# Optimization experiments

Measured on AMD Instinct MI355X. Metric: run time of the kernel, lower is better.

Reference implementation:

```python
import jax, jax.numpy as jnp
import numpy as np

C, N, NC, E, D, R = 16, 10000, 2000, 50000, 256, 32
NBLK = 3
IN_DIM = 4 + 134 + 6 * 4 + 18 * 4  # 234
EPS = 1e-5


def _instance_norm(x):
    # InstanceNorm1d (affine=False): normalize over the node axis per (config, channel)
    mu = jnp.mean(x, axis=1, keepdims=True)
    var = jnp.var(x, axis=1, keepdims=True)
    return (x - mu) * jax.lax.rsqrt(var + EPS)


def _channel_attn(x, W1, b1, W2, b2):
    t = jax.nn.relu(x @ W1 + b1)
    return jax.nn.sigmoid(t @ W2 + b2) * x


def setup_inputs() -> dict:
    key = jax.random.key(0)
    ks = jax.random.split(key, 24)
    sc = 0.05
    inp = {}
    inp["x_node_cfg"] = jax.random.randint(ks[0], (C, NC, 18), 0, 6)
    inp["x_feat"] = jax.random.normal(ks[1], (N, 134), jnp.float32)
    inp["x_node_layout_feat"] = jax.random.randint(ks[2], (N, 6), 0, 6)
    inp["x_op"] = jax.random.randint(ks[3], (N,), 0, 120)
    inp["edge_index"] = jax.random.randint(ks[4], (2, E), 0, N)
    inp["node_config_ids"] = jnp.arange(NC)
    # parameters
    inp["emb_op"] = jax.random.normal(ks[5], (120, 4)) * 0.1
    inp["emb_layout"] = jax.random.normal(ks[6], (8, 4)) * 0.1
    inp["lin1_W"] = jax.random.normal(ks[7], (IN_DIM, D)) * sc
    inp["lin1_b"] = jnp.full((D,), 0.01, jnp.float32)
    inp["ca1_W1"] = jax.random.normal(ks[8], (D, R)) * sc
    inp["ca1_b1"] = jnp.zeros((R,), jnp.float32)
    inp["ca1_W2"] = jax.random.normal(ks[9], (R, D)) * sc
    inp["ca1_b2"] = jnp.zeros((D,), jnp.float32)
    inp["lin2_W"] = jax.random.normal(ks[10], (D, D)) * sc
    inp["lin2_b"] = jnp.full((D,), 0.01, jnp.float32)
    inp["ca2_W1"] = jax.random.normal(ks[11], (D, R)) * sc
    inp["ca2_b1"] = jnp.zeros((R,), jnp.float32)
    inp["ca2_W2"] = jax.random.normal(ks[12], (R, D)) * sc
    inp["ca2_b2"] = jnp.zeros((D,), jnp.float32)
    inp["sage_Wl"] = jax.random.normal(ks[13], (NBLK, D, D)) * sc
    inp["sage_bl"] = jnp.zeros((NBLK, D), jnp.float32)
    inp["sage_Wr"] = jax.random.normal(ks[14], (NBLK, D, D)) * sc
    inp["sca_W1"] = jax.random.normal(ks[15], (NBLK, D, R)) * sc
    inp["sca_b1"] = jnp.zeros((NBLK, R), jnp.float32)
    inp["sca_W2"] = jax.random.normal(ks[16], (NBLK, R, D)) * sc
    inp["sca_b2"] = jnp.zeros((NBLK, D), jnp.float32)
    inp["cls_W"] = jax.random.normal(ks[17], (D, 1)) * sc
    inp["cls_b"] = jnp.zeros((1,), jnp.float32)
    return inp


def _forward(x_node_cfg, x_feat, x_node_layout_feat, x_op, edge_index, node_config_ids,
             emb_op, emb_layout, lin1_W, lin1_b, ca1_W1, ca1_b1, ca1_W2, ca1_b2,
             lin2_W, lin2_b, ca2_W1, ca2_b1, ca2_W2, ca2_b2,
             sage_Wl, sage_bl, sage_Wr, sca_W1, sca_b1, sca_W2, sca_b2, cls_W, cls_b):
    n_cfg = x_node_cfg.shape[0]
    n_nodes = x_feat.shape[0]
    # build per-node config feature: -2 fill, scatter configured nodes, shift by +2
    node_cfg = jnp.full((n_cfg, n_nodes, 18), -2, x_node_cfg.dtype)
    node_cfg = node_cfg.at[:, node_config_ids].set(x_node_cfg) + 2
    cfg_emb = emb_layout[node_cfg].reshape(n_cfg, n_nodes, 18 * 4)  # [C,N,72]
    layout_emb = emb_layout[x_node_layout_feat + 2].reshape(n_nodes, 6 * 4)  # [N,24]
    op_emb = emb_op[x_op]  # [N,4]
    feat = jnp.concatenate([
        jnp.broadcast_to(x_feat[None], (n_cfg, n_nodes, x_feat.shape[1])),
        cfg_emb,
        jnp.broadcast_to(layout_emb[None], (n_cfg, n_nodes, layout_emb.shape[1])),
        jnp.broadcast_to(op_emb[None], (n_cfg, n_nodes, op_emb.shape[1])),
    ], axis=2)  # [C,N,234]

    # LinearActNorm 1
    h = feat @ lin1_W + lin1_b
    h = _instance_norm(h)
    h = _channel_attn(h, ca1_W1, ca1_b1, ca1_W2, ca1_b2)
    h = jax.nn.gelu(h, approximate=False)
    # LinearActNorm 2
    h = h @ lin2_W + lin2_b
    h = _instance_norm(h)
    h = _channel_attn(h, ca2_W1, ca2_b1, ca2_W2, ca2_b2)
    h = jax.nn.gelu(h, approximate=False)

    src, tgt = edge_index[0], edge_index[1]
    cnt = jnp.zeros((n_nodes,), h.dtype).at[tgt].add(1.0)
    inv_cnt = (1.0 / jnp.maximum(cnt, 1.0))[None, :, None]
    for i in range(sage_Wl.shape[0]):
        shortcut = h
        x = _instance_norm(h)
        # SAGEConv: mean aggregation of source features at targets + root transform
        agg = jnp.zeros_like(x).at[:, tgt, :].add(x[:, src, :]) * inv_cnt
        x = agg @ sage_Wl[i] + sage_bl[i] + x @ sage_Wr[i]
        x = _channel_attn(x, sca_W1[i], sca_b1[i], sca_W2[i], sca_b2[i])
        h = jax.nn.gelu(x + shortcut, approximate=False)

    pooled = h.mean(axis=1)  # [C,D]
    return (pooled @ cls_W + cls_b).reshape(-1)  # [C]


def reference(x_node_cfg, x_feat, x_node_layout_feat, x_op, edge_index, node_config_ids,
              emb_op, emb_layout, lin1_W, lin1_b, ca1_W1, ca1_b1, ca1_W2, ca1_b2,
              lin2_W, lin2_b, ca2_W1, ca2_b1, ca2_W2, ca2_b2,
              sage_Wl, sage_bl, sage_Wr, sca_W1, sca_b1, sca_W2, sca_b2, cls_W, cls_b):
    return _forward(x_node_cfg, x_feat, x_node_layout_feat, x_op, edge_index, node_config_ids,
                    emb_op, emb_layout, lin1_W, lin1_b, ca1_W1, ca1_b1, ca1_W2, ca1_b2,
                    lin2_W, lin2_b, ca2_W1, ca2_b1, ca2_W2, ca2_b2,
                    sage_Wl, sage_bl, sage_Wr, sca_W1, sca_b1, sca_W2, sca_b2, cls_W, cls_b)
```

## Files before the change

### kernel.cpp

```cpp
#include <hip/hip_runtime.h>
#include <hip/hip_bf16.h>
#include <math.h>

constexpr int C_  = 16;
constexpr int N_  = 10000;
constexpr int NC_ = 2000;
constexpr int E_  = 50000;
constexpr int D_  = 256;
constexpr int SZ_ = N_ * D_;
constexpr float EPS_ = 1e-5f;

typedef unsigned short u16;
typedef __attribute__((ext_vector_type(8))) unsigned short us8v;
typedef __attribute__((ext_vector_type(4))) unsigned short us4v;
typedef __attribute__((ext_vector_type(8))) short s16x8;
typedef __attribute__((ext_vector_type(4))) float f32x4;

typedef __attribute__((address_space(3))) unsigned int lds_uint;
typedef const __attribute__((address_space(1))) unsigned int glb_uint;

__device__ __forceinline__ u16 f2bf(float f) {
    __hip_bfloat16 h = __float2bfloat16(f);
    return __builtin_bit_cast(u16, h);
}
__device__ __forceinline__ float bf2f(u16 h) {
    return __uint_as_float(((unsigned)h) << 16);
}
__device__ __forceinline__ float gelu_f(float x) {
    float z = x * 0.70710678118654752f;
    float az = fabsf(z);
    float t = 1.f / fmaf(0.3275911f, az, 1.f);
    float p = t * (0.254829592f + t * (-0.284496736f + t * (1.421413741f +
              t * (-1.453152027f + t * 1.061405429f))));
    float e = p * __expf(-z * z);
    float erfv = (z >= 0.f) ? (1.f - e) : (e - 1.f);
    return 0.5f * x * (1.f + erfv);
}


__global__ __launch_bounds__(256) void tbl_k(const float* __restrict__ embL,
                                             const float* __restrict__ W,
                                             float* __restrict__ T) {
    int b = blockIdx.x;
    int s = b >> 3, i = b & 7, d = threadIdx.x;
    float acc = 0.f;
#pragma unroll
    for (int k = 0; k < 4; ++k)
        acc = fmaf(embL[i * 4 + k], W[(134 + s * 4 + k) * 256 + d], acc);
    T[(s * 8 + i) * 256 + d] = acc;
}

__global__ __launch_bounds__(256) void csum_k(const float* __restrict__ T,
                                              float* __restrict__ cs) {
    int d = threadIdx.x;
    float a = 0.f;
#pragma unroll
    for (int s = 0; s < 18; ++s) a += T[(s * 8) * 256 + d];
    cs[d] = a;
}

__global__ __launch_bounds__(192) void feat_k(const float* __restrict__ xf,
                                              const int* __restrict__ xlay,
                                              const int* __restrict__ xop,
                                              const float* __restrict__ embL,
                                              const float* __restrict__ embO,
                                              float* __restrict__ f) {
    int n = blockIdx.x, j = threadIdx.x;
    if (j >= 176) return;
    float v;
    if (j < 134) v = xf[n * 134 + j];
    else if (j < 158) { int q = j - 134; int t = q >> 2, k = q & 3; v = embL[(xlay[n * 6 + t] + 2) * 4 + k]; }
    else if (j < 162) { int k = j - 158; v = embO[xop[n] * 4 + k]; }
    else v = 0.f;
    f[n * 176 + j] = v;
}

__global__ __launch_bounds__(256) void wpack_k(const float* __restrict__ W,
                                               float* __restrict__ Wp) {
    int j = blockIdx.x, d = threadIdx.x;
    float v = 0.f;
    if (j < 134) v = W[j * 256 + d];
    else if (j < 158) v = W[(206 + j - 134) * 256 + d];
    else if (j < 162) v = W[(230 + j - 158) * 256 + d];
    Wp[j * 256 + d] = v;
}

__global__ __launch_bounds__(256) void packw1_k(const float* __restrict__ W1,
                                                u16* __restrict__ dst) {
    int i = blockIdx.x * 256 + threadIdx.x;
    int j = i & 7, lane = (i >> 3) & 63, half = (i >> 9) & 1, ks = (i >> 10) & 1, wid = (i >> 11) & 3;
    int k = wid * 64 + ks * 32 + ((lane >> 4) << 3) + j;
    int col = half * 16 + (lane & 15);
    dst[i] = f2bf(W1[k * 32 + col]);
}
__global__ __launch_bounds__(256) void packw2_k(const float* __restrict__ W2,
                                                u16* __restrict__ dst) {
    int i = blockIdx.x * 256 + threadIdx.x;
    int j = i & 7, lane = (i >> 3) & 63, q = (i >> 9) & 3, wid = (i >> 11) & 3;
    int kq = lane >> 4, cl = lane & 15;
    dst[i] = f2bf(W2[(kq * 8 + j) * 256 + (wid * 4 + q) * 16 + cl]);
}

__global__ __launch_bounds__(256) void cfgpos_k(const int* __restrict__ ncid,
                                                int* __restrict__ cfgpos) {
    int i = blockIdx.x * 256 + threadIdx.x;
    if (i < NC_) cfgpos[ncid[i]] = i;
}

__global__ __launch_bounds__(256) void hist_k(const int* __restrict__ ei, int* __restrict__ cnt) {
    int e = blockIdx.x * 256 + threadIdx.x;
    if (e < E_) atomicAdd(&cnt[ei[E_ + e]], 1);
}

__global__ __launch_bounds__(1024) void scan_k(const int* __restrict__ cnt,
                                               int* __restrict__ off,
                                               int* __restrict__ cursor,
                                               float* __restrict__ invcnt) {
    __shared__ int s[1024];
    int t = threadIdx.x;
    int base = t * 10;
    int local[10];
    int part = 0;
#pragma unroll
    for (int k = 0; k < 10; ++k) {
        int idx = base + k;
        int v = (idx < N_) ? cnt[idx] : 0;
        local[k] = v; part += v;
    }
    s[t] = part;
    __syncthreads();
    for (int o = 1; o < 1024; o <<= 1) {
        int val = (t >= o) ? s[t - o] : 0;
        __syncthreads();
        s[t] += val;
        __syncthreads();
    }
    int pre = s[t] - part;
#pragma unroll
    for (int k = 0; k < 10; ++k) {
        int idx = base + k;
        if (idx < N_) {
            off[idx] = pre;
            cursor[idx] = pre;
            invcnt[idx] = 1.0f / (float)(local[k] > 1 ? local[k] : 1);
            pre += local[k];
        }
    }
    if (t == 1023) off[N_] = s[1023];
}

__global__ __launch_bounds__(256) void fill_k(const int* __restrict__ ei,
                                              int* __restrict__ cursor,
                                              int* __restrict__ csr) {
    int e = blockIdx.x * 256 + threadIdx.x;
    if (e < E_) {
        int t = ei[E_ + e];
        int p = atomicAdd(&cursor[t], 1);
        csr[p] = ei[e];
    }
}

__global__ __launch_bounds__(256) void wt2_k(const float* __restrict__ W,
                                             u16* __restrict__ Wt) {
    int j = blockIdx.x, k = threadIdx.x;
    Wt[j * 256 + k] = f2bf(W[k * 256 + j]);
}

__global__ __launch_bounds__(256) void foldw_k(const float* __restrict__ Wl,
                                               const float* __restrict__ Wr,
                                               const float* __restrict__ bl,
                                               const float* __restrict__ mu,
                                               const float* __restrict__ rs,
                                               u16* __restrict__ Wt,
                                               float* __restrict__ biasF) {
    __shared__ float red[256];
    int c = blockIdx.y, j = blockIdx.x, k = threadIdx.x;
    float rsv = rs[c * 256 + k], muv = mu[c * 256 + k];
    float fl = rsv * Wl[k * 256 + j];
    float fr = rsv * Wr[k * 256 + j];
    size_t wb = ((size_t)c * 256 + j) * 512;
    Wt[wb + k] = f2bf(fl);
    Wt[wb + 256 + k] = f2bf(fr);
    red[k] = muv * (fl + fr);
    __syncthreads();
    for (int s = 128; s > 0; s >>= 1) {
        if (k < s) red[k] += red[k + s];
        __syncthreads();
    }
    if (k == 0) biasF[c * 256 + j] = bl[j] - red[0];
}

__global__ __launch_bounds__(256) void lin1_cfg_k(const float* __restrict__ base,
                                                  const float* __restrict__ T,
                                                  const int* __restrict__ ncid,
                                                  const int* __restrict__ xcfg,
                                                  u16* __restrict__ H,
                                                  float* __restrict__ ssum,
                                                  float* __restrict__ ssq) {
    __shared__ int idxs[16][18];
    __shared__ int nid[16];
    const int c = blockIdx.z, j0 = blockIdx.x * 16, tid = threadIdx.x;
    if (tid < 16) nid[tid] = ncid[j0 + tid];
    for (int t = tid; t < 288; t += 256) {
        int row = t / 18, s = t - row * 18;
        idxs[row][s] = (xcfg[((size_t)c * NC_ + j0 + row) * 18 + s] + 2) * 256;
    }
    __syncthreads();
    const int d = tid;
    float psum = 0.f, psq = 0.f;
    for (int g = 0; g < 16; g += 4) {
        float acc[4];
#pragma unroll
        for (int gg = 0; gg < 4; ++gg) acc[gg] = base[(size_t)nid[g + gg] * 256 + d];
#pragma unroll
        for (int s = 0; s < 18; ++s) {
            const float* Ts = &T[s * 2048 + d];
#pragma unroll
            for (int gg = 0; gg < 4; ++gg)
                acc[gg] += Ts[idxs[g + gg][s]];
        }
#pragma unroll
        for (int gg = 0; gg < 4; ++gg) {
            H[((size_t)c * N_ + nid[g + gg]) * 256 + d] = f2bf(acc[gg]);
            psum += acc[gg]; psq += acc[gg] * acc[gg];
        }
    }
    atomicAdd(&ssum[c * 256 + d], psum);
    atomicAdd(&ssq[c * 256 + d], psq);
}

__global__ __launch_bounds__(256) void lin1_unc_k(const float* __restrict__ base,
                                                  const float* __restrict__ csum,
                                                  const int* __restrict__ cfgpos,
                                                  int nc,
                                                  u16* __restrict__ H,
                                                  float* __restrict__ ssum,
                                                  float* __restrict__ ssq) {
    __shared__ float red[2048];
    const int n0 = blockIdx.x * 16, tid = threadIdx.x;
    float ps[8] = {0, 0, 0, 0, 0, 0, 0, 0}, pq[8] = {0, 0, 0, 0, 0, 0, 0, 0};
#pragma unroll
    for (int it = 0; it < 2; ++it) {
        const int flat = tid + it * 256;
        const int row = flat >> 5, cb = (flat & 31) * 8;
        const int n = n0 + row;
        if (cfgpos[n] >= 0) continue;
        us8v b;
#pragma unroll
        for (int j = 0; j < 8; ++j) {
            float v = base[(size_t)n * 256 + cb + j] + csum[cb + j];
            b[j] = f2bf(v);
            ps[j] += v; pq[j] += v * v;
        }
        for (int c = 0; c < nc; ++c)
            *(us8v*)&H[((size_t)c * N_ + n) * 256 + cb] = b;
    }
#pragma unroll
    for (int j = 0; j < 8; ++j)
        red[((tid >> 5) * 32 + (tid & 31)) * 8 + j] = ps[j];
    __syncthreads();
    {
        const int cb2 = tid >> 3, j2 = tid & 7;
        float s = 0.f;
#pragma unroll
        for (int r8 = 0; r8 < 8; ++r8) s += red[(r8 * 32 + cb2) * 8 + j2];
        for (int c = 0; c < nc; ++c) atomicAdd(&ssum[c * 256 + tid], s);
    }
    __syncthreads();
#pragma unroll
    for (int j = 0; j < 8; ++j)
        red[((tid >> 5) * 32 + (tid & 31)) * 8 + j] = pq[j];
    __syncthreads();
    {
        const int cb2 = tid >> 3, j2 = tid & 7;
        float s = 0.f;
#pragma unroll
        for (int r8 = 0; r8 < 8; ++r8) s += red[(r8 * 32 + cb2) * 8 + j2];
        for (int c = 0; c < nc; ++c) atomicAdd(&ssq[c * 256 + tid], s);
    }
}

__global__ __launch_bounds__(256) void finstat_k(const float* __restrict__ ssum,
                                                 const float* __restrict__ ssq,
                                                 float* __restrict__ mu,
                                                 float* __restrict__ rs,
                                                 float* __restrict__ mrs) {
    int i = blockIdx.x * 256 + threadIdx.x;
    float m = ssum[i] * (1.0f / (float)N_);
    float v = ssq[i] * (1.0f / (float)N_) - m * m;
    float r = rsqrtf(v + EPS_);
    mu[i] = m;
    rs[i] = r;
    mrs[i] = m * r;
}

__global__ __launch_bounds__(256) void agg_k(const u16* __restrict__ H,
                                             const int* __restrict__ off,
                                             const int* __restrict__ csr,
                                             const float* __restrict__ invcnt,
                                             const float* __restrict__ mu,
                                             u16* __restrict__ Agg) {
    int wave = threadIdx.x >> 6, lane = threadIdx.x & 63;
    int pair = blockIdx.x * 4 + wave;
    int c = pair / N_, t = pair - c * N_;
    int d4 = lane * 4;
    int o0 = off[t], o1 = off[t + 1];
    int deg = o1 - o0;
    us4v o;
    if (deg > 0) {
        int myidx = (lane < deg) ? csr[o0 + lane] : 0;
        const u16* Hc = H + (size_t)c * SZ_ + d4;
        float ax = 0.f, ay = 0.f, az = 0.f, aw = 0.f;
        int lim = deg < 64 ? deg : 64;
        int i = 0;
        for (; i + 4 <= lim; i += 4) {
            int s0 = __shfl(myidx, i), s1 = __shfl(myidx, i + 1);
            int s2 = __shfl(myidx, i + 2), s3 = __shfl(myidx, i + 3);
            us4v h0 = *(const us4v*)&Hc[(size_t)s0 * 256];
            us4v h1 = *(const us4v*)&Hc[(size_t)s1 * 256];
            us4v h2 = *(const us4v*)&Hc[(size_t)s2 * 256];
            us4v h3 = *(const us4v*)&Hc[(size_t)s3 * 256];
            ax += (bf2f(h0.x) + bf2f(h1.x)) + (bf2f(h2.x) + bf2f(h3.x));
            ay += (bf2f(h0.y) + bf2f(h1.y)) + (bf2f(h2.y) + bf2f(h3.y));
            az += (bf2f(h0.z) + bf2f(h1.z)) + (bf2f(h2.z) + bf2f(h3.z));
            aw += (bf2f(h0.w) + bf2f(h1.w)) + (bf2f(h2.w) + bf2f(h3.w));
        }
        for (; i < lim; ++i) {
            int s = __shfl(myidx, i);
            us4v h = *(const us4v*)&Hc[(size_t)s * 256];
            ax += bf2f(h.x); ay += bf2f(h.y); az += bf2f(h.z); aw += bf2f(h.w);
        }
        for (int j = o0 + 64; j < o1; ++j) {
            int s = csr[j];
            us4v h = *(const us4v*)&Hc[(size_t)s * 256];
            ax += bf2f(h.x); ay += bf2f(h.y); az += bf2f(h.z); aw += bf2f(h.w);
        }
        float inv = invcnt[t];
        o.x = f2bf(ax * inv); o.y = f2bf(ay * inv);
        o.z = f2bf(az * inv); o.w = f2bf(aw * inv);
    } else {
        o.x = f2bf(mu[c * 256 + d4 + 0]);
        o.y = f2bf(mu[c * 256 + d4 + 1]);
        o.z = f2bf(mu[c * 256 + d4 + 2]);
        o.w = f2bf(mu[c * 256 + d4 + 3]);
    }
    *(us4v*)&Agg[((size_t)c * N_ + t) * 256 + d4] = o;
}

template <int STATS>
__global__ __launch_bounds__(256) void mgemm_k(
    const u16* __restrict__ A1, size_t sA1,
    const u16* __restrict__ A2, size_t sA2,
    const u16* __restrict__ Wt, size_t sW, int K1, int Ktot,
    const float* __restrict__ bias, size_t sBias,
    u16* __restrict__ Y, size_t sY, int Mrows,
    float* __restrict__ ssum, float* __restrict__ ssq)
{
    __shared__ u16 Asm[128 * 64];
    __shared__ u16 Bsm[128 * 64];
    const int tid = threadIdx.x;
    const int lane = tid & 63, wid = tid >> 6;
    const int wr = wid >> 1, wc = wid & 1;

    const int gx = gridDim.x, gy = gridDim.y;
    int nwg = gx * gy * gridDim.z;
    int orig = blockIdx.x + gx * (blockIdx.y + gy * blockIdx.z);
    int q = nwg >> 3, r = nwg & 7;
    int xcd = orig & 7, idx = orig >> 3;
    int swz = (xcd < r ? xcd * (q + 1) : r * (q + 1) + (xcd - r) * q) + idx;
    const int bx = swz % gx;
    const int tmp = swz / gx;
    const int by = tmp % gy;
    const int c  = tmp / gy;

    const int rowbase = by * 128, colbase = bx * 128;

    const u16* A1p = A1 + (size_t)c * sA1;
    const u16* A2p = A2 ? (A2 + (size_t)c * sA2) : nullptr;
    const u16* Wp  = Wt + (size_t)c * sW;

    f32x4 acc[4][4];
#pragma unroll
    for (int i = 0; i < 4; ++i)
#pragma unroll
        for (int j = 0; j < 4; ++j) acc[i][j] = (f32x4)0.f;

    const int lrow = lane >> 3;
    const int lchunk = lane & 7;

    for (int k0 = 0; k0 < Ktot; k0 += 64) {
        const u16* asrc; int ak;
        if (k0 < K1) { asrc = A1p; ak = k0; } else { asrc = A2p; ak = k0 - K1; }
#pragma unroll
        for (int i = 0; i < 4; ++i) {
            const int row = (wid * 4 + i) * 8 + lrow;
            const int srcchunk = lchunk ^ (row & 7);
            int garow = rowbase + row;
            if (garow >= Mrows) garow = Mrows - 1;
            const u16* ga = asrc + (size_t)garow * 256 + ak + srcchunk * 8;
            __builtin_amdgcn_global_load_lds((glb_uint*)ga,
                (lds_uint*)(Asm + (wid * 4 + i) * 512), 16, 0, 0);
            const u16* gb = Wp + (size_t)(colbase + row) * Ktot + k0 + srcchunk * 8;
            __builtin_amdgcn_global_load_lds((glb_uint*)gb,
                (lds_uint*)(Bsm + (wid * 4 + i) * 512), 16, 0, 0);
        }
        __syncthreads();
#pragma unroll
        for (int ks = 0; ks < 2; ++ks) {
            s16x8 aF[4], bF[4];
            const int kk = ks * 32 + ((lane >> 4) << 3);
#pragma unroll
            for (int f = 0; f < 4; ++f) {
                int ar = wr * 64 + f * 16 + (lane & 15);
                aF[f] = *(const s16x8*)&Asm[(ar * 64 + kk) ^ ((ar & 7) << 3)];
                int br = wc * 64 + f * 16 + (lane & 15);
                bF[f] = *(const s16x8*)&Bsm[(br * 64 + kk) ^ ((br & 7) << 3)];
            }
#pragma unroll
            for (int fr = 0; fr < 4; ++fr)
#pragma unroll
                for (int fc = 0; fc < 4; ++fc)
                    acc[fr][fc] = __builtin_amdgcn_mfma_f32_16x16x32_bf16(
                        aF[fr], bF[fc], acc[fr][fc], 0, 0, 0);
        }
        __syncthreads();
    }

    float bcol[4];
#pragma unroll
    for (int fc = 0; fc < 4; ++fc)
        bcol[fc] = bias[(size_t)c * sBias + colbase + wc * 64 + fc * 16 + (lane & 15)];
    u16* Yp = Y + (size_t)c * sY;
    float ps[4] = {0, 0, 0, 0}, pq[4] = {0, 0, 0, 0};
#pragma unroll
    for (int fr = 0; fr < 4; ++fr) {
#pragma unroll
        for (int i = 0; i < 4; ++i) {
            int grow = rowbase + wr * 64 + fr * 16 + ((lane >> 4) << 2) + i;
            if (grow < Mrows) {
                size_t rb = (size_t)grow * 256 + colbase + wc * 64 + (lane & 15);
#pragma unroll
                for (int fc = 0; fc < 4; ++fc) {
                    float v = acc[fr][fc][i] + bcol[fc];
                    Yp[rb + fc * 16] = f2bf(v);
                    if (STATS) { ps[fc] += v; pq[fc] += v * v; }
                }
            }
        }
    }
    if (STATS) {
#pragma unroll
        for (int fc = 0; fc < 4; ++fc) {
            float s = ps[fc], q2 = pq[fc];
            s += __shfl_xor(s, 16); s += __shfl_xor(s, 32);
            q2 += __shfl_xor(q2, 16); q2 += __shfl_xor(q2, 32);
            if (lane < 16) {
                int col = colbase + wc * 64 + fc * 16 + lane;
                atomicAdd(&ssum[c * 256 + col], s);
                atomicAdd(&ssq[c * 256 + col], q2);
            }
        }
    }
}

template <int SMODE>
__global__ __launch_bounds__(512) void msage_k(
    const u16* __restrict__ A1,
    const u16* __restrict__ A2,
    const u16* __restrict__ Wt, size_t sW,
    const float* __restrict__ biasF,
    const u16* __restrict__ W1p, const float* __restrict__ b1,
    const u16* __restrict__ W2p, const float* __restrict__ b2,
    u16* __restrict__ Yout, int Mrows,
    float* __restrict__ ssum, float* __restrict__ ssq)
{
    __shared__ __align__(16) char SM[81920];
    u16*   xbf = (u16*)SM;
    u16*   tbf = (u16*)(SM + 33792);
    float* red = (float*)SM;

    const int tid = threadIdx.x;
    const int lane = tid & 63, w = tid >> 6;
    const int cl = lane & 15, kq = lane >> 4;

    int nwg = gridDim.x * gridDim.y;
    int orig = blockIdx.x + gridDim.x * blockIdx.y;
    int q = nwg >> 3, r = nwg & 7;
    int xcd = orig & 7, idx = orig >> 3;
    int swz = (xcd < r ? xcd * (q + 1) : r * (q + 1) + (xcd - r) * q) + idx;
    const int by = swz % gridDim.x;
    const int c  = swz / gridDim.x;
    const int rowbase = by * 64;

    const u16* A1p = A1 + (size_t)c * SZ_;
    const u16* A2p = A2 + (size_t)c * SZ_;
    const u16* Wp  = Wt + (size_t)c * sW;

    f32x4 acc[4][2];
#pragma unroll
    for (int i = 0; i < 4; ++i)
#pragma unroll
        for (int j = 0; j < 2; ++j) acc[i][j] = (f32x4)0.f;

    auto stage = [&](int buf, int k0) {
        const u16* asrc = (k0 < 256) ? A1p : A2p;
        const int ak = (k0 < 256) ? k0 : (k0 - 256);
        u16* Ab = (u16*)(SM + buf * 40960);
        u16* Bb = (u16*)(SM + buf * 40960 + 8192);
        {
            const int u = tid;
            const int row = u >> 3, chunk = u & 7;
            const int sc2 = chunk ^ (row & 7);
            int garow = rowbase + row;
            if (garow >= Mrows) garow = Mrows - 1;
            __builtin_amdgcn_global_load_lds(
                (glb_uint*)(asrc + (size_t)garow * 256 + ak + sc2 * 8),
                (lds_uint*)(Ab + (w * 64) * 8), 16, 0, 0);
        }
#pragma unroll
        for (int jj = 0; jj < 4; ++jj) {
            const int u = tid + jj * 512;
            const int wcol = u >> 3, chunk = u & 7;
            const int sc2 = chunk ^ (wcol & 7);
            __builtin_amdgcn_global_load_lds(
                (glb_uint*)(Wp + (size_t)wcol * 512 + k0 + sc2 * 8),
                (lds_uint*)(Bb + (jj * 512 + w * 64) * 8), 16, 0, 0);
        }
    };

    stage(0, 0);
    __syncthreads();
    int cur = 0;
    for (int t = 0; t < 8; ++t) {
        if (t < 7) stage(cur ^ 1, (t + 1) * 64);
        const u16* Asm = (const u16*)(SM + cur * 40960);
        const u16* Bsm = (const u16*)(SM + cur * 40960 + 8192);
#pragma unroll
        for (int ks = 0; ks < 2; ++ks) {
            s16x8 aF[4], bF[2];
            const int kk = ks * 32 + kq * 8;
#pragma unroll
            for (int f = 0; f < 4; ++f) {
                const int ar = f * 16 + cl;
                aF[f] = *(const s16x8*)&Asm[(ar * 64 + kk) ^ ((ar & 7) << 3)];
            }
#pragma unroll
            for (int fc = 0; fc < 2; ++fc) {
                const int bc = w * 32 + fc * 16 + cl;
                bF[fc] = *(const s16x8*)&Bsm[(bc * 64 + kk) ^ ((bc & 7) << 3)];
            }
#pragma unroll
            for (int fr = 0; fr < 4; ++fr)
#pragma unroll
                for (int fc = 0; fc < 2; ++fc)
                    acc[fr][fc] = __builtin_amdgcn_mfma_f32_16x16x32_bf16(
                        aF[fr], bF[fc], acc[fr][fc], 0, 0, 0);
        }
        __syncthreads();
        cur ^= 1;
    }

    float bcol[2];
#pragma unroll
    for (int fc = 0; fc < 2; ++fc)
        bcol[fc] = biasF[c * 256 + w * 32 + fc * 16 + cl];

#pragma unroll
    for (int fr = 0; fr < 4; ++fr)
#pragma unroll
        for (int i = 0; i < 4; ++i) {
            const int rloc = fr * 16 + kq * 4 + i;
#pragma unroll
            for (int fc = 0; fc < 2; ++fc)
                xbf[rloc * 264 + w * 32 + fc * 16 + cl] =
                    f2bf(acc[fr][fc][i] + bcol[fc]);
        }
    __syncthreads();
    {
        const int rb = w >> 1, ch = w & 1;
        f32x4 at = (f32x4)0.f;
#pragma unroll
        for (int s = 0; s < 8; ++s) {
            s16x8 aF = *(const s16x8*)&xbf[(rb * 16 + cl) * 264 + s * 32 + kq * 8];
            s16x8 bF = *(const s16x8*)&W1p[((s * 2 + ch) * 64 + lane) * 8];
            at = __builtin_amdgcn_mfma_f32_16x16x32_bf16(aF, bF, at, 0, 0, 0);
        }
        const float b1v = b1[ch * 16 + cl];
#pragma unroll
        for (int i = 0; i < 4; ++i)
            tbf[(rb * 16 + kq * 4 + i) * 40 + ch * 16 + cl] =
                f2bf(fmaxf(at[i] + b1v, 0.f));
    }
    __syncthreads();
    {
        s16x8 aF[4];
#pragma unroll
        for (int rg = 0; rg < 4; ++rg)
            aF[rg] = *(const s16x8*)&tbf[(rg * 16 + cl) * 40 + kq * 8];
#pragma unroll
        for (int q2 = 0; q2 < 2; ++q2) {
            const int cf = w * 2 + q2;
            const int colb = cf * 16;
            s16x8 bF = *(const s16x8*)&W2p[(cf * 64 + lane) * 8];
            const float b2v = b2[colb + cl];
#pragma unroll
            for (int rg = 0; rg < 4; ++rg) {
                f32x4 a2 = __builtin_amdgcn_mfma_f32_16x16x32_bf16(
                    aF[rg], bF, (f32x4)0.f, 0, 0, 0);
#pragma unroll
                for (int i = 0; i < 4; ++i) {
                    const int ea = (rg * 16 + kq * 4 + i) * 264 + colb + cl;
                    float s = a2[i] + b2v;
                    float sig = 1.f / (1.f + __expf(-s));
                    xbf[ea] = f2bf(sig * bf2f(xbf[ea]));
                }
            }
        }
    }
    __syncthreads();
    float ps[8] = {0, 0, 0, 0, 0, 0, 0, 0}, pq[8] = {0, 0, 0, 0, 0, 0, 0, 0};
#pragma unroll
    for (int it = 0; it < 4; ++it) {
        const int e = tid + it * 512;
        const int row = e >> 5, cb = (e & 31) * 8;
        const int grow = rowbase + row;
        if (grow < Mrows) {
            us8v xv = *(const us8v*)&xbf[row * 264 + cb];
            us8v rv = *(const us8v*)&Yout[((size_t)c * N_ + grow) * 256 + cb];
            us8v ov;
#pragma unroll
            for (int j = 0; j < 8; ++j) {
                float v = gelu_f(bf2f(xv[j]) + bf2f(rv[j]));
                ov[j] = f2bf(v);
                ps[j] += v;
                if (SMODE == 1) pq[j] += v * v;
            }
            *(us8v*)&Yout[((size_t)c * N_ + grow) * 256 + cb] = ov;
        }
    }
    __syncthreads();
#pragma unroll
    for (int j = 0; j < 8; ++j)
        red[((tid >> 5) * 32 + (tid & 31)) * 8 + j] = ps[j];
    __syncthreads();
    if (tid < 256) {
        const int cb2 = tid >> 3, j2 = tid & 7;
        float s = 0.f;
#pragma unroll
        for (int r16 = 0; r16 < 16; ++r16) s += red[(r16 * 32 + cb2) * 8 + j2];
        atomicAdd(&ssum[c * 256 + cb2 * 8 + j2], s);
    }
    if (SMODE == 1) {
        __syncthreads();
#pragma unroll
        for (int j = 0; j < 8; ++j)
            red[((tid >> 5) * 32 + (tid & 31)) * 8 + j] = pq[j];
        __syncthreads();
        if (tid < 256) {
            const int cb2 = tid >> 3, j2 = tid & 7;
            float s = 0.f;
#pragma unroll
            for (int r16 = 0; r16 < 16; ++r16) s += red[(r16 * 32 + cb2) * 8 + j2];
            atomicAdd(&ssq[c * 256 + cb2 * 8 + j2], s);
        }
    }
}

__global__ __launch_bounds__(256) void gemm_k(const float* __restrict__ A1, int lda1,
                                              const float* __restrict__ W1, int K1,
                                              const float* __restrict__ bias,
                                              float* __restrict__ Y, int Mrows) {
    __shared__ float As[16][132];
    __shared__ float Bs[16][132];
    float acc[8][8];
#pragma unroll
    for (int i = 0; i < 8; ++i)
#pragma unroll
        for (int j = 0; j < 8; ++j) acc[i][j] = 0.f;

    const int tid = threadIdx.x;
    const int tr = tid >> 4, tc = tid & 15;
    const int rowbase = blockIdx.y * 128, colbase = blockIdx.x * 128;

    for (int k0 = 0; k0 < K1; k0 += 16) {
#pragma unroll
        for (int ii = 0; ii < 2; ++ii) {
            int i = tid + ii * 256;
            int rr = i >> 2, qq = i & 3;
            int grow = rowbase + rr;
            float4 vv = make_float4(0.f, 0.f, 0.f, 0.f);
            if (grow < Mrows) vv = *(const float4*)&A1[(size_t)grow * lda1 + k0 + qq * 4];
            As[qq * 4 + 0][rr] = vv.x;
            As[qq * 4 + 1][rr] = vv.y;
            As[qq * 4 + 2][rr] = vv.z;
            As[qq * 4 + 3][rr] = vv.w;
        }
#pragma unroll
        for (int ii = 0; ii < 2; ++ii) {
            int i = tid + ii * 256;
            int rr = i >> 5, qq = i & 31;
            float4 vv = *(const float4*)&W1[(size_t)(k0 + rr) * 256 + colbase + qq * 4];
            *(float4*)&Bs[rr][qq * 4] = vv;
        }
        __syncthreads();
#pragma unroll
        for (int kk = 0; kk < 16; ++kk) {
            float a[8], b[8];
            *(float4*)&a[0] = *(const float4*)&As[kk][tr * 4];
            *(float4*)&a[4] = *(const float4*)&As[kk][64 + tr * 4];
            *(float4*)&b[0] = *(const float4*)&Bs[kk][tc * 4];
            *(float4*)&b[4] = *(const float4*)&Bs[kk][64 + tc * 4];
#pragma unroll
            for (int i = 0; i < 8; ++i)
#pragma unroll
                for (int j = 0; j < 8; ++j)
                    acc[i][j] = fmaf(a[i], b[j], acc[i][j]);
        }
        __syncthreads();
    }

    float4 blo = *(const float4*)&bias[colbase + tc * 4];
    float4 bhi = *(const float4*)&bias[colbase + 64 + tc * 4];
    float bb[8] = {blo.x, blo.y, blo.z, blo.w, bhi.x, bhi.y, bhi.z, bhi.w};
#pragma unroll
    for (int i = 0; i < 8; ++i)
#pragma unroll
        for (int j = 0; j < 8; ++j) acc[i][j] += bb[j];

#pragma unroll
    for (int i = 0; i < 8; ++i) {
        int lrow = (i < 4) ? (tr * 4 + i) : (64 + tr * 4 + (i - 4));
        int grow = rowbase + lrow;
        if (grow < Mrows) {
            *(float4*)&Y[(size_t)grow * 256 + colbase + tc * 4] =
                make_float4(acc[i][0], acc[i][1], acc[i][2], acc[i][3]);
            *(float4*)&Y[(size_t)grow * 256 + colbase + 64 + tc * 4] =
                make_float4(acc[i][4], acc[i][5], acc[i][6], acc[i][7]);
        }
    }
}

template <int NORM, int RES, int SMODE>
__global__ __launch_bounds__(512) void apply_k(const u16* __restrict__ Yin,
                                               u16* __restrict__ Hout,
                                               const u16* __restrict__ Hsc,
                                               const u16* __restrict__ W1p,
                                               const float* __restrict__ b1,
                                               const u16* __restrict__ W2p,
                                               const float* __restrict__ b2,
                                               const float* __restrict__ rs,
                                               const float* __restrict__ mrs,
                                               float* __restrict__ ssum,
                                               float* __restrict__ ssq) {
    __shared__ u16 vbf[16 * 264];
    __shared__ u16 scs[(RES ? 16 : 1) * 264];
    __shared__ float tpart[8 * 528];
    __shared__ u16 tbf[16 * 40];
    __shared__ float srs[NORM ? 256 : 1], smrs[NORM ? 256 : 1];
    const int c = blockIdx.z, n0 = blockIdx.x * 16, tid = threadIdx.x;
    const int lane = tid & 63, wid = tid >> 6;
    const size_t rowbase = ((size_t)c * N_ + n0) * 256;

    if (NORM && tid < 256) { srs[tid] = rs[c * 256 + tid]; smrs[tid] = mrs[c * 256 + tid]; }
    {
        const int row = tid >> 5, cb = (tid & 31) * 8;
        us8v x = *(const us8v*)&Yin[rowbase + row * 256 + cb];
        us8v r;
        if (RES) r = *(const us8v*)&Hsc[rowbase + row * 256 + cb];
        if (NORM) {
            __syncthreads();
            us8v y;
#pragma unroll
            for (int j = 0; j < 8; ++j)
                y[j] = f2bf(fmaf(bf2f(x[j]), srs[cb + j], -smrs[cb + j]));
            *(us8v*)&vbf[row * 264 + cb] = y;
        } else {
            *(us8v*)&vbf[row * 264 + cb] = x;
        }
        if (RES) *(us8v*)&scs[row * 264 + cb] = r;
    }
    __syncthreads();

    {
        const int arow = lane & 15, kq = lane >> 4;
        const int k = wid * 32 + kq * 8;
        s16x8 aF = *(const s16x8*)&vbf[arow * 264 + k];
        s16x8 bF0 = *(const s16x8*)&W1p[((wid * 2 + 0) * 64 + lane) * 8];
        s16x8 bF1 = *(const s16x8*)&W1p[((wid * 2 + 1) * 64 + lane) * 8];
        f32x4 at0 = __builtin_amdgcn_mfma_f32_16x16x32_bf16(aF, bF0, (f32x4)0.f, 0, 0, 0);
        f32x4 at1 = __builtin_amdgcn_mfma_f32_16x16x32_bf16(aF, bF1, (f32x4)0.f, 0, 0, 0);
#pragma unroll
        for (int i = 0; i < 4; ++i) {
            tpart[wid * 528 + (kq * 4 + i) * 33 + (lane & 15)] = at0[i];
            tpart[wid * 528 + (kq * 4 + i) * 33 + 16 + (lane & 15)] = at1[i];
        }
    }
    __syncthreads();

    {
        const int nr = tid >> 5, col = tid & 31;
        float s = b1[col];
#pragma unroll
        for (int w8 = 0; w8 < 8; ++w8)
            s += tpart[w8 * 528 + nr * 33 + col];
        tbf[nr * 40 + col] = f2bf(fmaxf(s, 0.f));
    }
    __syncthreads();

    {
        const int cl = lane & 15, kq = lane >> 4;
        s16x8 aF = *(const s16x8*)&tbf[cl * 40 + kq * 8];
        float ps[2] = {0, 0}, pq[2] = {0, 0};
#pragma unroll
        for (int q = 0; q < 2; ++q) {
            const int colb = (wid * 2 + q) * 16;
            s16x8 bF = *(const s16x8*)&W2p[((wid * 2 + q) * 64 + lane) * 8];
            f32x4 acc = __builtin_amdgcn_mfma_f32_16x16x32_bf16(aF, bF, (f32x4)0.f, 0, 0, 0);
            const float b2v = b2[colb + cl];
#pragma unroll
            for (int i = 0; i < 4; ++i) {
                const int row = kq * 4 + i;
                const int ea = row * 264 + colb + cl;
                float s = acc[i] + b2v;
                float sig = 1.0f / (1.0f + __expf(-s));
                float val = sig * bf2f(vbf[ea]);
                if (RES) val += bf2f(scs[ea]);
                val = gelu_f(val);
                vbf[ea] = f2bf(val);
                if (SMODE) { ps[q] += val; if (SMODE == 1) pq[q] += val * val; }
            }
        }
        if (SMODE) {
#pragma unroll
            for (int q = 0; q < 2; ++q) {
                float s = ps[q];
                s += __shfl_xor(s, 16); s += __shfl_xor(s, 32);
                if (SMODE == 1) {
                    float q2 = pq[q];
                    q2 += __shfl_xor(q2, 16); q2 += __shfl_xor(q2, 32);
                    if (lane < 16) atomicAdd(&ssq[c * 256 + (wid * 2 + q) * 16 + lane], q2);
                }
                if (lane < 16) atomicAdd(&ssum[c * 256 + (wid * 2 + q) * 16 + lane], s);
            }
        }
    }
    __syncthreads();

    {
        const int row = tid >> 5, cb = (tid & 31) * 8;
        us8v h = *(const us8v*)&vbf[row * 264 + cb];
        *(us8v*)&Hout[rowbase + row * 256 + cb] = h;
    }
}

__global__ __launch_bounds__(256) void cls_k(const float* __restrict__ pooled_sum,
                                             const float* __restrict__ clsW,
                                             const float* __restrict__ clsb,
                                             float* __restrict__ out) {
    __shared__ float red[256];
    int c = blockIdx.x, d = threadIdx.x;
    red[d] = pooled_sum[c * 256 + d] * (1.0f / (float)N_) * clsW[d];
    __syncthreads();
    for (int s = 128; s > 0; s >>= 1) {
        if (d < s) red[d] += red[d + s];
        __syncthreads();
    }
    if (d == 0) out[c] = red[0] + clsb[0];
}

static inline size_t alup(size_t x) { return (x + 255) & ~(size_t)255; }

extern "C" void kernel_launch(void* const* d_in, const int* in_sizes, int n_in,
                              void* d_out, int out_size, void* d_ws, size_t ws_size,
                              hipStream_t stream) {
    const int*   xcfg   = (const int*)d_in[0];
    const float* xfeat  = (const float*)d_in[1];
    const int*   xlay   = (const int*)d_in[2];
    const int*   xop    = (const int*)d_in[3];
    const int*   ei     = (const int*)d_in[4];
    const int*   ncid   = (const int*)d_in[5];
    const float* embO   = (const float*)d_in[6];
    const float* embL   = (const float*)d_in[7];
    const float* lin1W  = (const float*)d_in[8];
    const float* lin1b  = (const float*)d_in[9];
    const float* ca1W1  = (const float*)d_in[10];
    const float* ca1b1  = (const float*)d_in[11];
    const float* ca1W2  = (const float*)d_in[12];
    const float* ca1b2  = (const float*)d_in[13];
    const float* lin2W  = (const float*)d_in[14];
    const float* lin2b  = (const float*)d_in[15];
    const float* ca2W1  = (const float*)d_in[16];
    const float* ca2b1  = (const float*)d_in[17];
    const float* ca2W2  = (const float*)d_in[18];
    const float* ca2b2  = (const float*)d_in[19];
    const float* sageWl = (const float*)d_in[20];
    const float* sagebl = (const float*)d_in[21];
    const float* sageWr = (const float*)d_in[22];
    const float* scaW1  = (const float*)d_in[23];
    const float* scab1  = (const float*)d_in[24];
    const float* scaW2  = (const float*)d_in[25];
    const float* scab2  = (const float*)d_in[26];
    const float* clsW   = (const float*)d_in[27];
    const float* clsb   = (const float*)d_in[28];
    float* out = (float*)d_out;

    char* w = (char*)d_ws;
    size_t o = 0;
    auto take = [&](size_t bytes) { char* p = w + o; o = alup(o + bytes); return p; };
    float* base    = (float*)take((size_t)N_ * 256 * 4);
    float* feat162 = (float*)take((size_t)N_ * 176 * 4);
    float* W162    = (float*)take((size_t)176 * 256 * 4);
    float* T       = (float*)take((size_t)18 * 8 * 256 * 4);
    float* csum    = (float*)take((size_t)256 * 4);
    float* stats   = (float*)take((size_t)6 * 8192 * 4);
    float* MU      = (float*)take((size_t)5 * 4096 * 4);
    float* RS      = (float*)take((size_t)5 * 4096 * 4);
    float* MRS     = (float*)take((size_t)5 * 4096 * 4);
    float* invcnt  = (float*)take((size_t)N_ * 4);
    int*   cnt     = (int*)take((size_t)N_ * 4);
    int*   off     = (int*)take((size_t)(N_ + 1) * 4);
    int*   cursor  = (int*)take((size_t)N_ * 4);
    int*   csr     = (int*)take((size_t)E_ * 4);
    int*   cfgpos  = (int*)take((size_t)N_ * 4);
    u16*   Wt2     = (u16*)take((size_t)256 * 256 * 2);
    u16*   Wfold   = (u16*)take((size_t)C_ * 256 * 512 * 2);
    float* biasF   = (float*)take((size_t)C_ * 256 * 4);
    u16*   CAW1    = (u16*)take((size_t)5 * 8192 * 2);
    u16*   CAW2    = (u16*)take((size_t)5 * 8192 * 2);

    const size_t slab = (size_t)SZ_ * 2;
    size_t avail = (ws_size > o) ? (ws_size - o) : 0;
    int Cc = (int)(avail / (3 * slab + 768));
    if (Cc > C_) Cc = C_;
    if (Cc < 1) Cc = 1;
    u16* BufH = (u16*)take((size_t)Cc * slab);
    u16* BufY = (u16*)take((size_t)Cc * slab);
    u16* BufA = (u16*)take((size_t)Cc * slab);
    (void)in_sizes; (void)n_in; (void)out_size;

    auto S = [&](int s) { return stats + (size_t)s * 8192; };
    auto Q = [&](int s) { return stats + (size_t)s * 8192 + 4096; };

    hipMemsetAsync(stats, 0, 6 * 8192 * 4, stream);
    hipMemsetAsync(cnt, 0, N_ * 4, stream);
    hipMemsetAsync(cfgpos, 0xFF, N_ * 4, stream);

    tbl_k<<<144, 256, 0, stream>>>(embL, lin1W, T);
    csum_k<<<1, 256, 0, stream>>>(T, csum);
    feat_k<<<N_, 192, 0, stream>>>(xfeat, xlay, xop, embL, embO, feat162);
    wpack_k<<<176, 256, 0, stream>>>(lin1W, W162);
    wt2_k<<<256, 256, 0, stream>>>(lin2W, Wt2);
    packw1_k<<<32, 256, 0, stream>>>(ca1W1, CAW1 + 0 * 8192);
    packw1_k<<<32, 256, 0, stream>>>(ca2W1, CAW1 + 1 * 8192);
    packw1_k<<<32, 256, 0, stream>>>(scaW1 + 0 * 8192, CAW1 + 2 * 8192);
    packw1_k<<<32, 256, 0, stream>>>(scaW1 + 1 * 8192, CAW1 + 3 * 8192);
    packw1_k<<<32, 256, 0, stream>>>(scaW1 + 2 * 8192, CAW1 + 4 * 8192);
    packw2_k<<<32, 256, 0, stream>>>(ca1W2, CAW2 + 0 * 8192);
    packw2_k<<<32, 256, 0, stream>>>(ca2W2, CAW2 + 1 * 8192);
    packw2_k<<<32, 256, 0, stream>>>(scaW2 + 0 * 8192, CAW2 + 2 * 8192);
    packw2_k<<<32, 256, 0, stream>>>(scaW2 + 1 * 8192, CAW2 + 3 * 8192);
    packw2_k<<<32, 256, 0, stream>>>(scaW2 + 2 * 8192, CAW2 + 4 * 8192);
    cfgpos_k<<<(NC_ + 255) / 256, 256, 0, stream>>>(ncid, cfgpos);
    hist_k<<<(E_ + 255) / 256, 256, 0, stream>>>(ei, cnt);
    scan_k<<<1, 1024, 0, stream>>>(cnt, off, cursor, invcnt);
    fill_k<<<(E_ + 255) / 256, 256, 0, stream>>>(ei, cursor, csr);

    gemm_k<<<dim3(2, 79, 1), 256, 0, stream>>>(feat162, 176, W162, 176, lin1b, base, N_);

    for (int c0 = 0; c0 < C_; c0 += Cc) {
        const int nc = (C_ - c0 < Cc) ? (C_ - c0) : Cc;
        const int co = c0 * 256;

        lin1_cfg_k<<<dim3(NC_ / 16, 1, nc), 256, 0, stream>>>(
            base, T, ncid, xcfg + (size_t)c0 * NC_ * 18, BufH, S(0) + co, Q(0) + co);
        lin1_unc_k<<<625, 256, 0, stream>>>(
            base, csum, cfgpos, nc, BufH, S(0) + co, Q(0) + co);
        finstat_k<<<nc, 256, 0, stream>>>(S(0) + co, Q(0) + co,
                                          MU + co, RS + co, MRS + co);

        apply_k<1, 0, 0><<<dim3(625, 1, nc), 512, 0, stream>>>(
            BufH, BufH, nullptr, CAW1 + 0 * 8192, ca1b1, CAW2 + 0 * 8192, ca1b2,
            RS + co, MRS + co, nullptr, nullptr);

        mgemm_k<1><<<dim3(2, 79, nc), 256, 0, stream>>>(
            BufH, SZ_, nullptr, 0, Wt2, 0, 256, 256,
            lin2b, 0, BufY, SZ_, N_, S(1) + co, Q(1) + co);
        finstat_k<<<nc, 256, 0, stream>>>(S(1) + co, Q(1) + co,
                                          MU + 4096 + co, RS + 4096 + co, MRS + 4096 + co);

        apply_k<1, 0, 1><<<dim3(625, 1, nc), 512, 0, stream>>>(
            BufY, BufY, nullptr, CAW1 + 1 * 8192, ca2b1, CAW2 + 1 * 8192, ca2b2,
            RS + 4096 + co, MRS + 4096 + co, S(2) + co, Q(2) + co);

        for (int i = 0; i < 3; ++i) {
            const int set = 2 + i;
            finstat_k<<<nc, 256, 0, stream>>>(S(set) + co, Q(set) + co,
                                              MU + set * 4096 + co, RS + set * 4096 + co,
                                              MRS + set * 4096 + co);
            foldw_k<<<dim3(256, nc), 256, 0, stream>>>(
                sageWl + (size_t)i * 65536, sageWr + (size_t)i * 65536, sagebl + i * 256,
                MU + set * 4096 + co, RS + set * 4096 + co,
                Wfold + (size_t)c0 * 256 * 512, biasF + co);
            agg_k<<<nc * 2500, 256, 0, stream>>>(BufY, off, csr, invcnt,
                                                 MU + set * 4096 + co, BufA);
            if (i < 2) {
                msage_k<1><<<dim3(157, nc), 512, 0, stream>>>(
                    BufA, BufY, Wfold + (size_t)c0 * 256 * 512, 256 * 512, biasF + co,
                    CAW1 + (2 + i) * 8192, scab1 + i * 32,
                    CAW2 + (2 + i) * 8192, scab2 + i * 256,
                    BufY, N_, S(3 + i) + co, Q(3 + i) + co);
            } else {
                msage_k<2><<<dim3(157, nc), 512, 0, stream>>>(
                    BufA, BufY, Wfold + (size_t)c0 * 256 * 512, 256 * 512, biasF + co,
                    CAW1 + (2 + i) * 8192, scab1 + i * 32,
                    CAW2 + (2 + i) * 8192, scab2 + i * 256,
                    BufY, N_, S(5) + co, nullptr);
            }
        }
    }

    cls_k<<<16, 256, 0, stream>>>(S(5), clsW, clsb, out);
}
```

Baseline: 1.169 ms.

## Fold instance-norm stat finalization into consumers and double-buffer mgemm LDS staging

Removes the separate finstat_k launches. Consumers (foldw_k, agg_k, apply_k) now compute mean and rsqrt variance directly from the raw sum and sum-of-squares buffers, which cuts several small kernel launches per chunk. The mgemm kernel also switches to a 64KB double-buffered LDS layout, so the next K-tile's global_load_lds runs while the current tile is being multiplied. The cost is redundant stat recomputation in each consumer block and more LDS per block, which may lower occupancy.

```diff
diff --git a/kernel.cpp b/kernel.cpp
--- a/kernel.cpp
+++ b/kernel.cpp
@@ -169,13 +169,16 @@
 __global__ __launch_bounds__(256) void foldw_k(const float* __restrict__ Wl,
                                                const float* __restrict__ Wr,
                                                const float* __restrict__ bl,
-                                               const float* __restrict__ mu,
-                                               const float* __restrict__ rs,
+                                               const float* __restrict__ nssum,
+                                               const float* __restrict__ nssq,
                                                u16* __restrict__ Wt,
                                                float* __restrict__ biasF) {
     __shared__ float red[256];
     int c = blockIdx.y, j = blockIdx.x, k = threadIdx.x;
-    float rsv = rs[c * 256 + k], muv = mu[c * 256 + k];
+    float m = nssum[c * 256 + k] * (1.0f / (float)N_);
+    float v = nssq[c * 256 + k] * (1.0f / (float)N_) - m * m;
+    float rsv = rsqrtf(v + EPS_);
+    float muv = m;
     float fl = rsv * Wl[k * 256 + j];
     float fr = rsv * Wr[k * 256 + j];
     size_t wb = ((size_t)c * 256 + j) * 512;
@@ -280,25 +283,11 @@
     }
 }
 
-__global__ __launch_bounds__(256) void finstat_k(const float* __restrict__ ssum,
-                                                 const float* __restrict__ ssq,
-                                                 float* __restrict__ mu,
-                                                 float* __restrict__ rs,
-                                                 float* __restrict__ mrs) {
-    int i = blockIdx.x * 256 + threadIdx.x;
-    float m = ssum[i] * (1.0f / (float)N_);
-    float v = ssq[i] * (1.0f / (float)N_) - m * m;
-    float r = rsqrtf(v + EPS_);
-    mu[i] = m;
-    rs[i] = r;
-    mrs[i] = m * r;
-}
-
 __global__ __launch_bounds__(256) void agg_k(const u16* __restrict__ H,
                                              const int* __restrict__ off,
                                              const int* __restrict__ csr,
                                              const float* __restrict__ invcnt,
-                                             const float* __restrict__ mu,
+                                             const float* __restrict__ nssum,
                                              u16* __restrict__ Agg) {
     int wave = threadIdx.x >> 6, lane = threadIdx.x & 63;
     int pair = blockIdx.x * 4 + wave;
@@ -339,10 +328,11 @@
         o.x = f2bf(ax * inv); o.y = f2bf(ay * inv);
         o.z = f2bf(az * inv); o.w = f2bf(aw * inv);
     } else {
-        o.x = f2bf(mu[c * 256 + d4 + 0]);
-        o.y = f2bf(mu[c * 256 + d4 + 1]);
-        o.z = f2bf(mu[c * 256 + d4 + 2]);
-        o.w = f2bf(mu[c * 256 + d4 + 3]);
+        const float invN = 1.0f / (float)N_;
+        o.x = f2bf(nssum[c * 256 + d4 + 0] * invN);
+        o.y = f2bf(nssum[c * 256 + d4 + 1] * invN);
+        o.z = f2bf(nssum[c * 256 + d4 + 2] * invN);
+        o.w = f2bf(nssum[c * 256 + d4 + 3] * invN);
     }
     *(us4v*)&Agg[((size_t)c * N_ + t) * 256 + d4] = o;
 }
@@ -356,8 +346,7 @@
     u16* __restrict__ Y, size_t sY, int Mrows,
     float* __restrict__ ssum, float* __restrict__ ssq)
 {
-    __shared__ u16 Asm[128 * 64];
-    __shared__ u16 Bsm[128 * 64];
+    __shared__ __align__(16) char SM[65536];
     const int tid = threadIdx.x;
     const int lane = tid & 63, wid = tid >> 6;
     const int wr = wid >> 1, wc = wid & 1;
@@ -385,26 +374,35 @@
 #pragma unroll
         for (int j = 0; j < 4; ++j) acc[i][j] = (f32x4)0.f;
 
-    const int lrow = lane >> 3;
-    const int lchunk = lane & 7;
-
-    for (int k0 = 0; k0 < Ktot; k0 += 64) {
+    auto stage = [&](int buf, int k0) {
         const u16* asrc; int ak;
         if (k0 < K1) { asrc = A1p; ak = k0; } else { asrc = A2p; ak = k0 - K1; }
-#pragma unroll
-        for (int i = 0; i < 4; ++i) {
-            const int row = (wid * 4 + i) * 8 + lrow;
-            const int srcchunk = lchunk ^ (row & 7);
+        u16* Ab = (u16*)(SM + buf * 32768);
+        u16* Bb = (u16*)(SM + buf * 32768 + 16384);
+#pragma unroll
+        for (int jj = 0; jj < 4; ++jj) {
+            const int u = tid + jj * 256;
+            const int row = u >> 3, chunk = u & 7;
+            const int sc2 = chunk ^ (row & 7);
             int garow = rowbase + row;
             if (garow >= Mrows) garow = Mrows - 1;
-            const u16* ga = asrc + (size_t)garow * 256 + ak + srcchunk * 8;
-            __builtin_amdgcn_global_load_lds((glb_uint*)ga,
-                (lds_uint*)(Asm + (wid * 4 + i) * 512), 16, 0, 0);
-            const u16* gb = Wp + (size_t)(colbase + row) * Ktot + k0 + srcchunk * 8;
-            __builtin_amdgcn_global_load_lds((glb_uint*)gb,
-                (lds_uint*)(Bsm + (wid * 4 + i) * 512), 16, 0, 0);
-        }
-        __syncthreads();
+            __builtin_amdgcn_global_load_lds(
+                (glb_uint*)(asrc + (size_t)garow * 256 + ak + sc2 * 8),
+                (lds_uint*)(Ab + u * 8), 16, 0, 0);
+            __builtin_amdgcn_global_load_lds(
+                (glb_uint*)(Wp + (size_t)(colbase + row) * Ktot + k0 + sc2 * 8),
+                (lds_uint*)(Bb + u * 8), 16, 0, 0);
+        }
+    };
+
+    const int nsteps = Ktot >> 6;
+    stage(0, 0);
+    __syncthreads();
+    int cur = 0;
+    for (int t = 0; t < nsteps; ++t) {
+        if (t + 1 < nsteps) stage(cur ^ 1, (t + 1) * 64);
+        const u16* Asm = (const u16*)(SM + cur * 32768);
+        const u16* Bsm = (const u16*)(SM + cur * 32768 + 16384);
 #pragma unroll
         for (int ks = 0; ks < 2; ++ks) {
             s16x8 aF[4], bF[4];
@@ -424,6 +422,7 @@
                         aF[fr], bF[fc], acc[fr][fc], 0, 0, 0);
         }
         __syncthreads();
+        cur ^= 1;
     }
 
     float bcol[4];
@@ -748,8 +747,8 @@
                                                const float* __restrict__ b1,
                                                const u16* __restrict__ W2p,
                                                const float* __restrict__ b2,
-                                               const float* __restrict__ rs,
-                                               const float* __restrict__ mrs,
+                                               const float* __restrict__ nssum,
+                                               const float* __restrict__ nssq,
                                                float* __restrict__ ssum,
                                                float* __restrict__ ssq) {
     __shared__ u16 vbf[16 * 264];
@@ -761,7 +760,13 @@
     const int lane = tid & 63, wid = tid >> 6;
     const size_t rowbase = ((size_t)c * N_ + n0) * 256;
 
-    if (NORM && tid < 256) { srs[tid] = rs[c * 256 + tid]; smrs[tid] = mrs[c * 256 + tid]; }
+    if (NORM && tid < 256) {
+        float m = nssum[c * 256 + tid] * (1.0f / (float)N_);
+        float v = nssq[c * 256 + tid] * (1.0f / (float)N_) - m * m;
+        float r = rsqrtf(v + EPS_);
+        srs[tid] = r;
+        smrs[tid] = m * r;
+    }
     {
         const int row = tid >> 5, cb = (tid & 31) * 8;
         us8v x = *(const us8v*)&Yin[rowbase + row * 256 + cb];
@@ -913,9 +918,6 @@
     float* T       = (float*)take((size_t)18 * 8 * 256 * 4);
     float* csum    = (float*)take((size_t)256 * 4);
     float* stats   = (float*)take((size_t)6 * 8192 * 4);
-    float* MU      = (float*)take((size_t)5 * 4096 * 4);
-    float* RS      = (float*)take((size_t)5 * 4096 * 4);
-    float* MRS     = (float*)take((size_t)5 * 4096 * 4);
     float* invcnt  = (float*)take((size_t)N_ * 4);
     int*   cnt     = (int*)take((size_t)N_ * 4);
     int*   off     = (int*)take((size_t)(N_ + 1) * 4);
@@ -975,34 +977,27 @@
             base, T, ncid, xcfg + (size_t)c0 * NC_ * 18, BufH, S(0) + co, Q(0) + co);
         lin1_unc_k<<<625, 256, 0, stream>>>(
             base, csum, cfgpos, nc, BufH, S(0) + co, Q(0) + co);
-        finstat_k<<<nc, 256, 0, stream>>>(S(0) + co, Q(0) + co,
-                                          MU + co, RS + co, MRS + co);
 
         apply_k<1, 0, 0><<<dim3(625, 1, nc), 512, 0, stream>>>(
             BufH, BufH, nullptr, CAW1 + 0 * 8192, ca1b1, CAW2 + 0 * 8192, ca1b2,
-            RS + co, MRS + co, nullptr, nullptr);
+            S(0) + co, Q(0) + co, nullptr, nullptr);
 
         mgemm_k<1><<<dim3(2, 79, nc), 256, 0, stream>>>(
             BufH, SZ_, nullptr, 0, Wt2, 0, 256, 256,
             lin2b, 0, BufY, SZ_, N_, S(1) + co, Q(1) + co);
-        finstat_k<<<nc, 256, 0, stream>>>(S(1) + co, Q(1) + co,
-                                          MU + 4096 + co, RS + 4096 + co, MRS + 4096 + co);
 
         apply_k<1, 0, 1><<<dim3(625, 1, nc), 512, 0, stream>>>(
             BufY, BufY, nullptr, CAW1 + 1 * 8192, ca2b1, CAW2 + 1 * 8192, ca2b2,
-            RS + 4096 + co, MRS + 4096 + co, S(2) + co, Q(2) + co);
+            S(1) + co, Q(1) + co, S(2) + co, Q(2) + co);
 
         for (int i = 0; i < 3; ++i) {
             const int set = 2 + i;
-            finstat_k<<<nc, 256, 0, stream>>>(S(set) + co, Q(set) + co,
-                                              MU + set * 4096 + co, RS + set * 4096 + co,
-                                              MRS + set * 4096 + co);
             foldw_k<<<dim3(256, nc), 256, 0, stream>>>(
                 sageWl + (size_t)i * 65536, sageWr + (size_t)i * 65536, sagebl + i * 256,
-                MU + set * 4096 + co, RS + set * 4096 + co,
+                S(set) + co, Q(set) + co,
                 Wfold + (size_t)c0 * 256 * 512, biasF + co);
             agg_k<<<nc * 2500, 256, 0, stream>>>(BufY, off, csr, invcnt,
-                                                 MU + set * 4096 + co, BufA);
+                                                 S(set) + co, BufA);
             if (i < 2) {
                 msage_k<1><<<dim3(157, nc), 512, 0, stream>>>(
                     BufA, BufY, Wfold + (size_t)c0 * 256 * 512, 256 * 512, biasF + co,
```

Result: faster. 1.143 ms (-2.3%).
